# Kernel tuning notes

Hardware: AMD Instinct MI355X
Metric: run time of the kernel (lower is better)

## Reference

```python
import jax, jax.numpy as jnp
import numpy as np

N_HEADS = 8
KEY_DIM = 16
VALUE_DIM = 16
EMBED = N_HEADS * KEY_DIM  # 128
B, N = 32, 16384


def setup_inputs() -> dict:
    key = jax.random.key(0)
    k1, k2, k3, k4 = jax.random.split(key, 4)
    query = jax.random.normal(k1, (B, 1, EMBED), dtype=jnp.float32)
    keys = jax.random.normal(k2, (B, 1, N, EMBED), dtype=jnp.float32)
    values = jax.random.normal(k3, (B, 1, N, EMBED), dtype=jnp.float32)
    mask = jnp.zeros((B, 1, N), dtype=jnp.float32)  # additive mask
    W_out = jax.random.normal(k4, (N_HEADS * VALUE_DIM, EMBED), dtype=jnp.float32) * 0.05
    return {"query": query, "keys": keys, "values": values, "mask": mask, "W_out": W_out}


def _make_heads(v, d):
    # [B, N, H*d] -> [H, B, N, d]
    b, n, _ = v.shape
    return jnp.transpose(v.reshape(b, n, N_HEADS, d), (2, 0, 1, 3))


def reference(query, keys, values, mask, W_out):
    k = keys[:, 0]    # [B, N, E]
    v = values[:, 0]  # [B, N, E]
    q = _make_heads(query, KEY_DIM)   # [H, B, 1, dk]
    K = _make_heads(k, KEY_DIM)       # [H, B, N, dk]
    V = _make_heads(v, VALUE_DIM)     # [H, B, N, dv]
    scale = jnp.float32(KEY_DIM) ** 0.5
    attn = jnp.einsum('hbqd,hbnd->hbqn', q, K) / scale  # [H, B, 1, N]
    attn = attn + mask                                   # broadcast [B,1,N]
    attn = jax.nn.softmax(attn, axis=-1)
    heads = jnp.einsum('hbqn,hbnd->hbqd', attn, V)       # [H, B, 1, dv]
    b = heads.shape[1]
    concat = jnp.transpose(heads, (1, 2, 0, 3)).reshape(b, 1, N_HEADS * VALUE_DIM)
    return concat @ W_out  # [B, 1, E]
```

## Files before the change

kernel.cpp:

```cpp
#include <hip/hip_runtime.h>
#include <math.h>

#define NHEADS 8
#define KD 16
#define EMBED 128
#define BATCH 32
#define NSEQ 16384
#define NCHUNK 64
#define CHUNK (NSEQ / NCHUNK)
#define PART_STRIDE 18

__global__ __launch_bounds__(256) void attn_partial(
    const float* __restrict__ q,
    const float* __restrict__ K,
    const float* __restrict__ V,
    const float* __restrict__ mask,
    float* __restrict__ part)
{
    const int b    = blockIdx.x >> 6;
    const int c    = blockIdx.x & 63;
    const int wave = threadIdx.x >> 6;
    const int lane = threadIdx.x & 63;
    const int head = lane >> 3;
    const int g    = lane & 7;

    const float2 q2 = *(const float2*)&q[b * EMBED + 2 * lane];

    float m = -INFINITY;
    float lsum = 0.f;
    float accx = 0.f, accy = 0.f;

    const size_t rowbase = (size_t)b * NSEQ;
    const int r0 = c * CHUNK;

    #pragma unroll 4
    for (int r = r0 + wave; r < r0 + CHUNK; r += 4) {
        const size_t off = (rowbase + r) * EMBED + 2 * lane;
        const float2 k2 = *(const float2*)&K[off];
        float p = q2.x * k2.x + q2.y * k2.y;
        p += __shfl_xor(p, 1);
        p += __shfl_xor(p, 2);
        p += __shfl_xor(p, 4);
        const float s  = p * 0.25f + mask[rowbase + r];
        const float mn = fmaxf(m, s);
        const float corr = __expf(m - mn);
        const float w    = __expf(s - mn);
        const float2 v2 = *(const float2*)&V[off];
        lsum = lsum * corr + w;
        accx = accx * corr + w * v2.x;
        accy = accy * corr + w * v2.y;
        m = mn;
    }

    __shared__ float lds[4][NHEADS][PART_STRIDE];
    lds[wave][head][2 + 2 * g]     = accx;
    lds[wave][head][2 + 2 * g + 1] = accy;
    if (g == 0) {
        lds[wave][head][0] = m;
        lds[wave][head][1] = lsum;
    }
    __syncthreads();

    const int t = threadIdx.x;
    if (t < EMBED) {
        const int h = t >> 4;
        const int d = t & 15;
        float M = -INFINITY;
        #pragma unroll
        for (int w = 0; w < 4; ++w) M = fmaxf(M, lds[w][h][0]);
        float L = 0.f, A = 0.f;
        #pragma unroll
        for (int w = 0; w < 4; ++w) {
            const float e = __expf(lds[w][h][0] - M);
            L += lds[w][h][1] * e;
            A += lds[w][h][2 + d] * e;
        }
        float* p = &part[((size_t)(b * NCHUNK + c) * NHEADS + h) * PART_STRIDE];
        p[2 + d] = A;
        if (d == 0) { p[0] = M; p[1] = L; }
    }
}

__global__ __launch_bounds__(128) void attn_finish(
    const float* __restrict__ part,
    const float* __restrict__ Wout,
    float* __restrict__ out)
{
    const int b = blockIdx.x;
    const int t = threadIdx.x;
    const int h = t >> 4;
    const int d = t & 15;

    __shared__ float heads[EMBED];

    float M = -INFINITY, L = 0.f, A = 0.f;
    for (int c = 0; c < NCHUNK; ++c) {
        const float* p = &part[((size_t)(b * NCHUNK + c) * NHEADS + h) * PART_STRIDE];
        const float mc = p[0];
        const float Mn = fmaxf(M, mc);
        const float eM = __expf(M - Mn);
        const float ec = __expf(mc - Mn);
        L = L * eM + p[1] * ec;
        A = A * eM + p[2 + d] * ec;
        M = Mn;
    }
    heads[t] = A / L;
    __syncthreads();

    float o = 0.f;
    #pragma unroll 8
    for (int dd = 0; dd < EMBED; ++dd)
        o += heads[dd] * Wout[dd * EMBED + t];
    out[b * EMBED + t] = o;
}

extern "C" void kernel_launch(void* const* d_in, const int* in_sizes, int n_in,
                              void* d_out, int out_size, void* d_ws, size_t ws_size,
                              hipStream_t stream) {
    const float* q    = (const float*)d_in[0];
    const float* K    = (const float*)d_in[1];
    const float* V    = (const float*)d_in[2];
    const float* mask = (const float*)d_in[3];
    const float* Wout = (const float*)d_in[4];
    float* out  = (float*)d_out;
    float* part = (float*)d_ws;

    attn_partial<<<BATCH * NCHUNK, 256, 0, stream>>>(q, K, V, mask, part);
    attn_finish<<<BATCH, 128, 0, stream>>>(part, Wout, out);
}
```

Measured before the change: 108.9 us.

## Use float4 loads with half-wave rows, contiguous per-wave row blocks and shuffled mask

Each wave now handles a contiguous block of 64 rows, two rows per iteration (one per half-wave), and each lane loads float4 from K and V instead of float2. The head dot product needs one fewer shuffle step. The mask is loaded once per wave as a coalesced vector and broadcast with a shuffle instead of one scalar load per row. The aim is wider, more coalesced memory traffic and fewer instructions per row, at the cost of twice as many online-softmax states to merge in LDS and somewhat more register pressure.

```diff
diff --git a/kernel.cpp b/kernel.cpp
--- a/kernel.cpp
+++ b/kernel.cpp
@@ -21,44 +21,51 @@
     const int c    = blockIdx.x & 63;
     const int wave = threadIdx.x >> 6;
     const int lane = threadIdx.x & 63;
-    const int head = lane >> 3;
-    const int g    = lane & 7;
+    const int half = lane >> 5;
+    const int lc   = lane & 31;
+    const int head = lc >> 2;
+    const int g    = lc & 3;
 
-    const float2 q2 = *(const float2*)&q[b * EMBED + 2 * lane];
+    const float4 q4 = *(const float4*)&q[b * EMBED + 4 * lc];
+
+    const size_t rowbase = (size_t)b * NSEQ;
+    const int rw = c * CHUNK + wave * 64;
+
+    const float mv = mask[rowbase + rw + lane];
 
     float m = -INFINITY;
     float lsum = 0.f;
-    float accx = 0.f, accy = 0.f;
-
-    const size_t rowbase = (size_t)b * NSEQ;
-    const int r0 = c * CHUNK;
+    float4 acc = {0.f, 0.f, 0.f, 0.f};
 
     #pragma unroll 4
-    for (int r = r0 + wave; r < r0 + CHUNK; r += 4) {
-        const size_t off = (rowbase + r) * EMBED + 2 * lane;
-        const float2 k2 = *(const float2*)&K[off];
-        float p = q2.x * k2.x + q2.y * k2.y;
+    for (int i = 0; i < 32; ++i) {
+        const int row = rw + 2 * i + half;
+        const size_t off = (rowbase + row) * EMBED + 4 * lc;
+        const float4 k4 = *(const float4*)&K[off];
+        const float4 v4 = *(const float4*)&V[off];
+        float p = q4.x * k4.x + q4.y * k4.y + q4.z * k4.z + q4.w * k4.w;
         p += __shfl_xor(p, 1);
         p += __shfl_xor(p, 2);
-        p += __shfl_xor(p, 4);
-        const float s  = p * 0.25f + mask[rowbase + r];
+        const float s  = p * 0.25f + __shfl(mv, 2 * i + half);
         const float mn = fmaxf(m, s);
         const float corr = __expf(m - mn);
         const float w    = __expf(s - mn);
-        const float2 v2 = *(const float2*)&V[off];
-        lsum = lsum * corr + w;
-        accx = accx * corr + w * v2.x;
-        accy = accy * corr + w * v2.y;
+        lsum  = lsum  * corr + w;
+        acc.x = acc.x * corr + w * v4.x;
+        acc.y = acc.y * corr + w * v4.y;
+        acc.z = acc.z * corr + w * v4.z;
+        acc.w = acc.w * corr + w * v4.w;
         m = mn;
     }
 
-    __shared__ float lds[4][NHEADS][PART_STRIDE];
-    lds[wave][head][2 + 2 * g]     = accx;
-    lds[wave][head][2 + 2 * g + 1] = accy;
-    if (g == 0) {
-        lds[wave][head][0] = m;
-        lds[wave][head][1] = lsum;
-    }
+    __shared__ float lds[8][NHEADS][PART_STRIDE];
+    const int set = wave * 2 + half;
+    float* dst = lds[set][head];
+    dst[2 + 4 * g + 0] = acc.x;
+    dst[2 + 4 * g + 1] = acc.y;
+    dst[2 + 4 * g + 2] = acc.z;
+    dst[2 + 4 * g + 3] = acc.w;
+    if (g == 0) { dst[0] = m; dst[1] = lsum; }
     __syncthreads();
 
     const int t = threadIdx.x;
@@ -67,13 +74,13 @@
         const int d = t & 15;
         float M = -INFINITY;
         #pragma unroll
-        for (int w = 0; w < 4; ++w) M = fmaxf(M, lds[w][h][0]);
+        for (int s8 = 0; s8 < 8; ++s8) M = fmaxf(M, lds[s8][h][0]);
         float L = 0.f, A = 0.f;
         #pragma unroll
-        for (int w = 0; w < 4; ++w) {
-            const float e = __expf(lds[w][h][0] - M);
-            L += lds[w][h][1] * e;
-            A += lds[w][h][2 + d] * e;
+        for (int s8 = 0; s8 < 8; ++s8) {
+            const float e = __expf(lds[s8][h][0] - M);
+            L += lds[s8][h][1] * e;
+            A += lds[s8][h][2 + d] * e;
         }
         float* p = &part[((size_t)(b * NCHUNK + c) * NHEADS + h) * PART_STRIDE];
         p[2 + d] = A;
```

Result: slower. 116.1 us (+6.6%).
